# Kernel tuning notes

Measured on AMD Instinct MI355X. Metric: run time of the kernel, lower is better.

The kernel has to match this reference:

```python
import jax, jax.numpy as jnp
import numpy as np

N = 12000       # nodes (Hi-C bins, max_num_nodes)
F_IN = 16       # number_genomic_annotations
HID = 4 * F_IN  # conv1 out = 64
NCLUST = 100    # n_clust
E = 384000      # edges (avg degree 32)


def setup_inputs() -> dict:
    key = jax.random.key(0)
    ks = jax.random.split(key, 8)
    x = jax.random.normal(ks[0], (N, F_IN), dtype=jnp.float32)
    edge_index = jax.random.randint(ks[1], (2, E), 0, N)
    edge_attr = jax.random.uniform(ks[2], (E,), dtype=jnp.float32)
    s1 = 1.0 / np.sqrt(F_IN)
    W1_rel = jax.random.uniform(ks[3], (HID, F_IN), minval=-s1, maxval=s1, dtype=jnp.float32)
    W1_root = jax.random.uniform(ks[4], (HID, F_IN), minval=-s1, maxval=s1, dtype=jnp.float32)
    b1 = jnp.zeros((HID,), jnp.float32)
    s2 = 1.0 / np.sqrt(HID)
    W2_rel = jax.random.uniform(ks[5], (NCLUST, HID), minval=-s2, maxval=s2, dtype=jnp.float32)
    W2_root = jax.random.uniform(ks[6], (NCLUST, HID), minval=-s2, maxval=s2, dtype=jnp.float32)
    b2 = jnp.zeros((NCLUST,), jnp.float32)
    return dict(x=x, edge_index=edge_index, edge_attr=edge_attr,
                W1_rel=W1_rel, W1_root=W1_root, b1=b1,
                W2_rel=W2_rel, W2_root=W2_root, b2=b2)


def _graph_conv(x, src, dst, ew, W_rel, W_root, b):
    # PyG GraphConv (aggr='add'): out = lin_rel(sum_j e_ji * x_j) + lin_root(x)
    msg = x[src] * ew[:, None]                       # [E, F]
    aggr = jax.ops.segment_sum(msg, dst, num_segments=N)  # [N, F]
    return aggr @ W_rel.T + b + x @ W_root.T


def reference(x, edge_index, edge_attr, W1_rel, W1_root, b1, W2_rel, W2_root, b2):
    src, dst = edge_index[0], edge_index[1]
    h = _graph_conv(x, src, dst, edge_attr, W1_rel, W1_root, b1)
    h = jax.nn.relu(h)  # dropout is identity in eval mode
    s_out = _graph_conv(h, src, dst, edge_attr, W2_rel, W2_root, b2)  # [N, NCLUST]

    # to_dense_adj (duplicate edges summed)
    adj = jnp.zeros((N, N), x.dtype).at[src, dst].add(edge_attr)  # [N, N]

    # dense_mincut_pool with S = x (as in the original forward), k = F_IN
    s_mc = jax.nn.softmax(x, axis=-1)      # [N, F_IN]
    as_ = adj @ s_mc                        # [N, F_IN]
    out_adj = s_mc.T @ as_                  # [F_IN, F_IN]
    mincut_num = jnp.trace(out_adj)
    d_flat = adj.sum(-1)                    # [N] degree
    mincut_den = jnp.einsum('ik,i,ik->', s_mc, d_flat, s_mc)  # trace(S^T D S)
    mc = -(mincut_num / mincut_den)

    ss = s_mc.T @ s_mc                      # [F_IN, F_IN]
    i_k = jnp.eye(F_IN, dtype=ss.dtype)
    o = jnp.linalg.norm(ss / jnp.linalg.norm(ss) - i_k / jnp.linalg.norm(i_k))

    return jax.nn.softmax(s_out, axis=-1), mc, o
```

## Files before the change

kernel.cpp:

```cpp
#include <hip/hip_runtime.h>
#include <math.h>

#define N_NODES 12000
#define F_INN 16
#define HIDD 64
#define NCLUST 100
#define NEDGE 384000
#define NBLK_N 47
#define CAP 96
#define EPT 4
#define NBLK_E 375
#define NBLK_F2 (N_NODES / 8)
#define NBIN 188
#define BINW 64
#define BCAP 2560
#define STCAP 24

#define OFF_BINCNT  0
#define OFF_SCAL    188
#define ZERO_ELEMS  190
#define OFF_COUNT   192
#define OFF_SSPART  12192
#define OFF_NORM2   24224
#define OFF_W2TREL  36224
#define OFF_W2TROOT 42624
#define OFF_SMC     49024
#define OFF_H       241024
#define OFF_SRCW    1009024
#define OFF_BINBUF  3313024

__global__ void binA_kernel(const float* __restrict__ x, const int* __restrict__ ei,
                            const float* __restrict__ ew, float* __restrict__ smc,
                            float* __restrict__ norm2, int* __restrict__ bincnt,
                            int2* __restrict__ binbuf, const float* __restrict__ W2_rel,
                            const float* __restrict__ W2_root, float* __restrict__ w2t_rel,
                            float* __restrict__ w2t_root) {
    __shared__ int shmA[188 + 188 * STCAP * 2];
    int t = threadIdx.x;
    int b = blockIdx.x;
    if (b < NBLK_E) {
        int* scnt = shmA;
        int2* sbuf = (int2*)(shmA + 188);
        for (int i = t; i < 188; i += 256) scnt[i] = 0;
        __syncthreads();
        int tid = b * 256 + t;
        int e0 = tid * EPT;
        int4 sv = *(const int4*)(ei + e0);
        int4 dv = *(const int4*)(ei + NEDGE + e0);
        float4 wv = *(const float4*)(ew + e0);
        int s[EPT] = {sv.x, sv.y, sv.z, sv.w};
        int d[EPT] = {dv.x, dv.y, dv.z, dv.w};
        float w[EPT] = {wv.x, wv.y, wv.z, wv.w};
#pragma unroll
        for (int i = 0; i < EPT; ++i) {
            int bin = d[i] >> 6;
            int dl = d[i] & 63;
            int2 rec = make_int2(s[i] | (dl << 16), __float_as_int(w[i]));
            int pos = atomicAdd(&scnt[bin], 1);
            if (pos < STCAP) {
                sbuf[bin * STCAP + pos] = rec;
            } else {
                int base = atomicAdd(&bincnt[bin], 1);
                binbuf[bin * BCAP + base] = rec;
            }
        }
        __syncthreads();
        if (t < 188) {
            int k = scnt[t];
            if (k > STCAP) k = STCAP;
            if (k > 0) {
                int base = atomicAdd(&bincnt[t], k);
                for (int i = 0; i < k; ++i) binbuf[t * BCAP + base + i] = sbuf[t * STCAP + i];
            }
        }
    } else if (b < NBLK_E + NBLK_N) {
        int i = (b - NBLK_E) * 256 + t;
        if (i >= N_NODES) return;
        const float4* xr = (const float4*)(x + i * 16);
        float4 r0 = xr[0], r1 = xr[1], r2 = xr[2], r3 = xr[3];
        float v[16] = {r0.x, r0.y, r0.z, r0.w, r1.x, r1.y, r1.z, r1.w,
                       r2.x, r2.y, r2.z, r2.w, r3.x, r3.y, r3.z, r3.w};
        float m = v[0];
#pragma unroll
        for (int k = 1; k < 16; ++k) m = fmaxf(m, v[k]);
        float s = 0.f;
#pragma unroll
        for (int k = 0; k < 16; ++k) { v[k] = __expf(v[k] - m); s += v[k]; }
        float inv = 1.f / s;
        float n2 = 0.f;
#pragma unroll
        for (int k = 0; k < 16; ++k) { v[k] *= inv; n2 += v[k] * v[k]; }
        float4* so = (float4*)(smc + i * 16);
        so[0] = make_float4(v[0], v[1], v[2], v[3]);
        so[1] = make_float4(v[4], v[5], v[6], v[7]);
        so[2] = make_float4(v[8], v[9], v[10], v[11]);
        so[3] = make_float4(v[12], v[13], v[14], v[15]);
        norm2[i] = n2;
    } else {
        float* fl = (float*)shmA;
        const float* src = (b == NBLK_E + NBLK_N) ? W2_rel : W2_root;
        float* dst = (b == NBLK_E + NBLK_N) ? w2t_rel : w2t_root;
        for (int i = t; i < 6400; i += 256) fl[i] = src[i];
        __syncthreads();
        for (int j = t; j < 6400; j += 256) {
            int kk = j / 100, cl = j - kk * 100;
            dst[j] = fl[cl * 64 + kk];
        }
    }
}

__global__ void binBF1_kernel(const int2* __restrict__ binbuf, const int* __restrict__ bincnt,
                              int* __restrict__ count, int2* __restrict__ srcw,
                              const float* __restrict__ x, const float* __restrict__ W1_rel,
                              const float* __restrict__ W1_root, const float* __restrict__ b1,
                              float* __restrict__ h, const float* __restrict__ smc,
                              float* __restrict__ sspart, const int* __restrict__ ei,
                              const float* __restrict__ ew, const float* __restrict__ norm2,
                              float* __restrict__ scal) {
    __shared__ int shmU[64 + 64 * CAP * 2];
    __shared__ float wrelT[1024], wrootT[1024], b1s[64];
    int t = threadIdx.x;
    int b = blockIdx.x;
    if (b < NBIN) {
        int* cnt = shmU;
        int2* lbuck = (int2*)(shmU + 64);
        for (int idx = t; idx < 1024; idx += 256) {
            int f = idx >> 4, k = idx & 15;
            wrelT[(k << 6) + f]  = W1_rel[idx];
            wrootT[(k << 6) + f] = W1_root[idx];
        }
        if (t < 64) b1s[t] = b1[t];
        for (int i = t; i < 64; i += 256) cnt[i] = 0;
        __syncthreads();
        int nE = bincnt[b];
        const int2* bp = binbuf + b * BCAP;
        for (int i = t; i < nE; i += 256) {
            int2 rec = bp[i];
            int src = rec.x & 0xFFFF;
            int dl = rec.x >> 16;
            int pos = atomicAdd(&cnt[dl], 1);
            if (pos < CAP) lbuck[dl * CAP + pos] = make_int2(src, rec.y);
        }
        __syncthreads();
        int nbase = b * BINW;
        int nvalid = N_NODES - nbase;
        if (nvalid > BINW) nvalid = BINW;
        if (t < nvalid) count[nbase + t] = cnt[t];
        int lim = nvalid * CAP;
        int2* outp = srcw + (size_t)nbase * CAP;
        for (int i = t; i < lim; i += 256) outp[i] = lbuck[i];
        int w = t >> 6, lane = t & 63;
        int j2 = lane >> 2;
        int q  = lane & 3;
        for (int ni = w; ni < nvalid; ni += 4) {
            int n = nbase + ni;
            int len = cnt[ni];
            const int2* bucket = lbuck + ni * CAP;
            float4 acc4 = make_float4(0.f, 0.f, 0.f, 0.f);
            for (int k = 0; k < len; k += 32) {
                int ia = k + j2, ib = k + 16 + j2;
                int2 pa = bucket[ia];
                int2 pb = bucket[ib];
                if (ia >= len) pa = make_int2(0, 0);
                if (ib >= len) pb = make_int2(0, 0);
                float4 va = *(const float4*)(x + pa.x * 16 + q * 4);
                float4 vb = *(const float4*)(x + pb.x * 16 + q * 4);
                float wa = __int_as_float(pa.y), wb = __int_as_float(pb.y);
                acc4.x = fmaf(va.x, wa, acc4.x); acc4.y = fmaf(va.y, wa, acc4.y);
                acc4.z = fmaf(va.z, wa, acc4.z); acc4.w = fmaf(va.w, wa, acc4.w);
                acc4.x = fmaf(vb.x, wb, acc4.x); acc4.y = fmaf(vb.y, wb, acc4.y);
                acc4.z = fmaf(vb.z, wb, acc4.z); acc4.w = fmaf(vb.w, wb, acc4.w);
            }
            acc4.x += __shfl_xor(acc4.x, 4);  acc4.y += __shfl_xor(acc4.y, 4);
            acc4.z += __shfl_xor(acc4.z, 4);  acc4.w += __shfl_xor(acc4.w, 4);
            acc4.x += __shfl_xor(acc4.x, 8);  acc4.y += __shfl_xor(acc4.y, 8);
            acc4.z += __shfl_xor(acc4.z, 8);  acc4.w += __shfl_xor(acc4.w, 8);
            acc4.x += __shfl_xor(acc4.x, 16); acc4.y += __shfl_xor(acc4.y, 16);
            acc4.z += __shfl_xor(acc4.z, 16); acc4.w += __shfl_xor(acc4.w, 16);
            acc4.x += __shfl_xor(acc4.x, 32); acc4.y += __shfl_xor(acc4.y, 32);
            acc4.z += __shfl_xor(acc4.z, 32); acc4.w += __shfl_xor(acc4.w, 32);
            float xv = (lane < 16) ? x[n * 16 + lane] : 0.f;
            float o = b1s[lane];
#define F1STEP(KK, COMP) { float ag = __shfl(acc4.COMP, (KK) >> 2);            \
                           float xb = __shfl(xv, (KK));                        \
                           o = fmaf(ag, wrelT[((KK) << 6) + lane],             \
                                    fmaf(xb, wrootT[((KK) << 6) + lane], o)); }
            F1STEP(0, x)  F1STEP(1, y)  F1STEP(2, z)  F1STEP(3, w)
            F1STEP(4, x)  F1STEP(5, y)  F1STEP(6, z)  F1STEP(7, w)
            F1STEP(8, x)  F1STEP(9, y)  F1STEP(10, z) F1STEP(11, w)
            F1STEP(12, x) F1STEP(13, y) F1STEP(14, z) F1STEP(15, w)
#undef F1STEP
            h[n * 64 + lane] = fmaxf(o, 0.f);
        }
    } else if (b < NBIN + NBLK_N) {
        int bb = b - NBIN;
        float* rows = (float*)shmU;
        int n = bb * 256 + t;
        float* rp = rows + t * 17;
        if (n < N_NODES) {
            const float4* sr = (const float4*)(smc + n * 16);
            float4 a0 = sr[0], a1 = sr[1], a2v = sr[2], a3 = sr[3];
            rp[0] = a0.x;  rp[1] = a0.y;  rp[2] = a0.z;  rp[3] = a0.w;
            rp[4] = a1.x;  rp[5] = a1.y;  rp[6] = a1.z;  rp[7] = a1.w;
            rp[8] = a2v.x; rp[9] = a2v.y; rp[10] = a2v.z; rp[11] = a2v.w;
            rp[12] = a3.x; rp[13] = a3.y; rp[14] = a3.z; rp[15] = a3.w;
        } else {
#pragma unroll
            for (int k = 0; k < 16; ++k) rp[k] = 0.f;
        }
        __syncthreads();
        int a = t & 15, bq = t >> 4;
        float accs = 0.f;
#pragma unroll 4
        for (int r = 0; r < 256; ++r)
            accs = fmaf(rows[r * 17 + a], rows[r * 17 + bq], accs);
        sspart[bb * 256 + t] = accs;
    } else {
        int tid = (b - NBIN - NBLK_N) * 256 + t;
        int e0 = tid * EPT;
        int4 sv = *(const int4*)(ei + e0);
        int4 dv = *(const int4*)(ei + NEDGE + e0);
        float4 wv = *(const float4*)(ew + e0);
        int s[EPT] = {sv.x, sv.y, sv.z, sv.w};
        int d[EPT] = {dv.x, dv.y, dv.z, dv.w};
        float w[EPT] = {wv.x, wv.y, wv.z, wv.w};
        float np = 0.f, dp = 0.f;
#pragma unroll
        for (int i = 0; i < EPT; ++i) {
            const float4* ps = (const float4*)(smc + s[i] * 16);
            const float4* pd = (const float4*)(smc + d[i] * 16);
            float4 s0 = ps[0], s1 = ps[1], s2 = ps[2], s3 = ps[3];
            float4 d0 = pd[0], d1 = pd[1], d2 = pd[2], d3 = pd[3];
            float dot = s0.x * d0.x + s0.y * d0.y + s0.z * d0.z + s0.w * d0.w +
                        s1.x * d1.x + s1.y * d1.y + s1.z * d1.z + s1.w * d1.w +
                        s2.x * d2.x + s2.y * d2.y + s2.z * d2.z + s2.w * d2.w +
                        s3.x * d3.x + s3.y * d3.y + s3.z * d3.z + s3.w * d3.w;
            np = fmaf(w[i], dot, np);
            dp = fmaf(w[i], norm2[s[i]], dp);
        }
        float* redn = (float*)shmU;
        float* redd = (float*)shmU + 256;
        redn[t] = np;
        redd[t] = dp;
        __syncthreads();
        for (int s2 = 128; s2 > 0; s2 >>= 1) {
            if (t < s2) { redn[t] += redn[t + s2]; redd[t] += redd[t + s2]; }
            __syncthreads();
        }
        if (t == 0) {
            atomicAdd(&scal[0], redn[0]);
            atomicAdd(&scal[1], redd[0]);
        }
    }
}

__global__ __launch_bounds__(512) void fused2_finalize_kernel(
    const float* __restrict__ h, const int2* __restrict__ srcw, const int* __restrict__ count,
    const float* __restrict__ w2t_rel, const float* __restrict__ w2t_root,
    const float* __restrict__ b2, float* __restrict__ out, const float* __restrict__ sspart,
    const float* __restrict__ scal) {
    __shared__ float wsrel[6400];
    __shared__ float a2[8][64], hrow[8][64];
    __shared__ float logits[8][104];
    __shared__ float b2s[104];
    int t = threadIdx.x;
    int b = blockIdx.x;
    if (b < NBLK_F2) {
        for (int i = t; i < 6400; i += 512) wsrel[i] = w2t_rel[i];
        if (t < NCLUST) b2s[t] = b2[t];
        int nn = t >> 6;
        int c = t & 63;
        int eslot = c >> 4;
        int q = c & 15;
        int n = b * 8 + nn;
        int len = count[n];
        const int2* bucket = srcw + n * CAP;
        float4 acc4 = make_float4(0.f, 0.f, 0.f, 0.f);
        for (int k = 0; k < len; k += 32) {
            int i0 = k + eslot,      i1 = k + 4 + eslot;
            int i2 = k + 8 + eslot,  i3 = k + 12 + eslot;
            int i4 = k + 16 + eslot, i5 = k + 20 + eslot;
            int i6 = k + 24 + eslot, i7 = k + 28 + eslot;
            int2 pa = bucket[i0]; int2 pb = bucket[i1];
            int2 pc = bucket[i2]; int2 pd = bucket[i3];
            int2 pe = bucket[i4]; int2 pf = bucket[i5];
            int2 pg = bucket[i6]; int2 ph = bucket[i7];
            if (i0 >= len) pa = make_int2(0, 0);
            if (i1 >= len) pb = make_int2(0, 0);
            if (i2 >= len) pc = make_int2(0, 0);
            if (i3 >= len) pd = make_int2(0, 0);
            if (i4 >= len) pe = make_int2(0, 0);
            if (i5 >= len) pf = make_int2(0, 0);
            if (i6 >= len) pg = make_int2(0, 0);
            if (i7 >= len) ph = make_int2(0, 0);
            float4 va = *(const float4*)(h + pa.x * 64 + q * 4);
            float4 vb = *(const float4*)(h + pb.x * 64 + q * 4);
            float4 vc = *(const float4*)(h + pc.x * 64 + q * 4);
            float4 vd = *(const float4*)(h + pd.x * 64 + q * 4);
            float4 ve = *(const float4*)(h + pe.x * 64 + q * 4);
            float4 vf = *(const float4*)(h + pf.x * 64 + q * 4);
            float4 vg = *(const float4*)(h + pg.x * 64 + q * 4);
            float4 vh = *(const float4*)(h + ph.x * 64 + q * 4);
            float wa = __int_as_float(pa.y), wb = __int_as_float(pb.y);
            float wc = __int_as_float(pc.y), wd = __int_as_float(pd.y);
            float we = __int_as_float(pe.y), wf = __int_as_float(pf.y);
            float wg = __int_as_float(pg.y), wh = __int_as_float(ph.y);
            acc4.x = fmaf(va.x, wa, acc4.x); acc4.y = fmaf(va.y, wa, acc4.y);
            acc4.z = fmaf(va.z, wa, acc4.z); acc4.w = fmaf(va.w, wa, acc4.w);
            acc4.x = fmaf(vb.x, wb, acc4.x); acc4.y = fmaf(vb.y, wb, acc4.y);
            acc4.z = fmaf(vb.z, wb, acc4.z); acc4.w = fmaf(vb.w, wb, acc4.w);
            acc4.x = fmaf(vc.x, wc, acc4.x); acc4.y = fmaf(vc.y, wc, acc4.y);
            acc4.z = fmaf(vc.z, wc, acc4.z); acc4.w = fmaf(vc.w, wc, acc4.w);
            acc4.x = fmaf(vd.x, wd, acc4.x); acc4.y = fmaf(vd.y, wd, acc4.y);
            acc4.z = fmaf(vd.z, wd, acc4.z); acc4.w = fmaf(vd.w, wd, acc4.w);
            acc4.x = fmaf(ve.x, we, acc4.x); acc4.y = fmaf(ve.y, we, acc4.y);
            acc4.z = fmaf(ve.z, we, acc4.z); acc4.w = fmaf(ve.w, we, acc4.w);
            acc4.x = fmaf(vf.x, wf, acc4.x); acc4.y = fmaf(vf.y, wf, acc4.y);
            acc4.z = fmaf(vf.z, wf, acc4.z); acc4.w = fmaf(vf.w, wf, acc4.w);
            acc4.x = fmaf(vg.x, wg, acc4.x); acc4.y = fmaf(vg.y, wg, acc4.y);
            acc4.z = fmaf(vg.z, wg, acc4.z); acc4.w = fmaf(vg.w, wg, acc4.w);
            acc4.x = fmaf(vh.x, wh, acc4.x); acc4.y = fmaf(vh.y, wh, acc4.y);
            acc4.z = fmaf(vh.z, wh, acc4.z); acc4.w = fmaf(vh.w, wh, acc4.w);
        }
        acc4.x += __shfl_xor(acc4.x, 16); acc4.y += __shfl_xor(acc4.y, 16);
        acc4.z += __shfl_xor(acc4.z, 16); acc4.w += __shfl_xor(acc4.w, 16);
        acc4.x += __shfl_xor(acc4.x, 32); acc4.y += __shfl_xor(acc4.y, 32);
        acc4.z += __shfl_xor(acc4.z, 32); acc4.w += __shfl_xor(acc4.w, 32);
        if (eslot == 0) *(float4*)(&a2[nn][q * 4]) = acc4;
        hrow[nn][c] = h[n * 64 + c];
        __syncthreads();
        int g = t >> 7, c2 = t & 127;
        if (c2 < NCLUST) {
            int na = 2 * g, nb2 = 2 * g + 1;
            float s0 = b2s[c2], s1 = s0;
#pragma unroll 8
            for (int kk = 0; kk < 64; ++kk) {
                float wr = wsrel[kk * 100 + c2];
                float wo = w2t_root[kk * 100 + c2];
                s0 = fmaf(a2[na][kk], wr, fmaf(hrow[na][kk], wo, s0));
                s1 = fmaf(a2[nb2][kk], wr, fmaf(hrow[nb2][kk], wo, s1));
            }
            logits[na][c2] = s0;
            logits[nb2][c2] = s1;
        }
        __syncthreads();
        float v0 = logits[nn][c];
        float v1 = (c < NCLUST - 64) ? logits[nn][64 + c] : -INFINITY;
        float m = fmaxf(v0, v1);
#pragma unroll
        for (int off = 32; off > 0; off >>= 1) m = fmaxf(m, __shfl_xor(m, off));
        float e0 = __expf(v0 - m);
        float e1 = (c < NCLUST - 64) ? __expf(v1 - m) : 0.f;
        float s = e0 + e1;
#pragma unroll
        for (int off = 32; off > 0; off >>= 1) s += __shfl_xor(s, off);
        float inv = 1.f / s;
        out[n * NCLUST + c] = e0 * inv;
        if (c < NCLUST - 64) out[n * NCLUST + 64 + c] = e1 * inv;
    } else {
        float* red = wsrel;
        float sv = 0.f;
        if (t < 256)
            for (int bb = 0; bb < NBLK_N; ++bb) sv += sspart[bb * 256 + t];
        red[t] = sv * sv;
        __syncthreads();
        for (int s = 256; s > 0; s >>= 1) {
            if (t < s) red[t] += red[t + s];
            __syncthreads();
        }
        float ssnorm = sqrtf(red[0]);
        __syncthreads();
        float diff = (t < 256) ? (sv / ssnorm - ((t % 17 == 0) ? 0.25f : 0.f)) : 0.f;
        red[t] = diff * diff;
        __syncthreads();
        for (int s = 256; s > 0; s >>= 1) {
            if (t < s) red[t] += red[t + s];
            __syncthreads();
        }
        if (t == 0) {
            out[N_NODES * NCLUST + 0] = -(scal[0] / scal[1]);
            out[N_NODES * NCLUST + 1] = sqrtf(red[0]);
        }
    }
}

extern "C" void kernel_launch(void* const* d_in, const int* in_sizes, int n_in,
                              void* d_out, int out_size, void* d_ws, size_t ws_size,
                              hipStream_t stream) {
    const float* x       = (const float*)d_in[0];
    const int*   ei      = (const int*)d_in[1];
    const float* ew      = (const float*)d_in[2];
    const float* W1_rel  = (const float*)d_in[3];
    const float* W1_root = (const float*)d_in[4];
    const float* b1      = (const float*)d_in[5];
    const float* W2_rel  = (const float*)d_in[6];
    const float* W2_root = (const float*)d_in[7];
    const float* b2      = (const float*)d_in[8];
    float* out = (float*)d_out;
    int*   wsi = (int*)d_ws;

    int*   bincnt  = wsi + OFF_BINCNT;
    float* scal    = (float*)(wsi + OFF_SCAL);
    int*   count   = wsi + OFF_COUNT;
    float* sspart  = (float*)(wsi + OFF_SSPART);
    float* norm2   = (float*)(wsi + OFF_NORM2);
    float* w2trel  = (float*)(wsi + OFF_W2TREL);
    float* w2troot = (float*)(wsi + OFF_W2TROOT);
    float* smc     = (float*)(wsi + OFF_SMC);
    float* h       = (float*)(wsi + OFF_H);
    int2*  srcw    = (int2*)(wsi + OFF_SRCW);
    int2*  binbuf  = (int2*)(wsi + OFF_BINBUF);

    hipMemsetAsync(wsi, 0, ZERO_ELEMS * sizeof(int), stream);
    binA_kernel<<<NBLK_E + NBLK_N + 2, 256, 0, stream>>>(x, ei, ew, smc, norm2, bincnt, binbuf,
                                                         W2_rel, W2_root, w2trel, w2troot);
    binBF1_kernel<<<NBIN + NBLK_N + NBLK_E, 256, 0, stream>>>(
        binbuf, bincnt, count, srcw, x, W1_rel, W1_root, b1, h,
        smc, sspart, ei, ew, norm2, scal);
    fused2_finalize_kernel<<<NBLK_F2 + 1, 512, 0, stream>>>(h, srcw, count, w2trel, w2troot,
                                                            b2, out, sspart, scal);
}
```

Baseline: 92.32 us.

## Drop materialized per-node edge buckets; rebuild buckets per 8-node block from bins

Removes the global srcw/count CSR-like bucket arrays. Each 8-node block in both conv kernels now scans its 64-node bin and keeps the edges belonging to its own 8 nodes in shared memory. This cuts global writes and reads of the bucket array and raises parallelism for conv1 from 188 bins to 1500 blocks of 512 threads. The cost is that each bin's records are read 8 times per conv stage, plus atomics on 8 shared counters.

```diff
diff --git a/kernel.cpp b/kernel.cpp
--- a/kernel.cpp
+++ b/kernel.cpp
@@ -8,8 +8,11 @@
 #define NEDGE 384000
 #define NBLK_N 47
 #define CAP 96
+#define LCAP 97
 #define EPT 4
 #define NBLK_E 375
+#define NBLK_F1 (N_NODES / 8)
+#define NBLK_ME 188
 #define NBLK_F2 (N_NODES / 8)
 #define NBIN 188
 #define BINW 64
@@ -19,15 +22,13 @@
 #define OFF_BINCNT  0
 #define OFF_SCAL    188
 #define ZERO_ELEMS  190
-#define OFF_COUNT   192
-#define OFF_SSPART  12192
-#define OFF_NORM2   24224
-#define OFF_W2TREL  36224
-#define OFF_W2TROOT 42624
-#define OFF_SMC     49024
-#define OFF_H       241024
-#define OFF_SRCW    1009024
-#define OFF_BINBUF  3313024
+#define OFF_SSPART  192
+#define OFF_NORM2   12224
+#define OFF_W2TREL  24224
+#define OFF_W2TROOT 30624
+#define OFF_SMC     37024
+#define OFF_H       229024
+#define OFF_BINBUF  997024
 
 __global__ void binA_kernel(const float* __restrict__ x, const int* __restrict__ ei,
                             const float* __restrict__ ew, float* __restrict__ smc,
@@ -109,141 +110,141 @@
     }
 }
 
-__global__ void binBF1_kernel(const int2* __restrict__ binbuf, const int* __restrict__ bincnt,
-                              int* __restrict__ count, int2* __restrict__ srcw,
-                              const float* __restrict__ x, const float* __restrict__ W1_rel,
-                              const float* __restrict__ W1_root, const float* __restrict__ b1,
-                              float* __restrict__ h, const float* __restrict__ smc,
-                              float* __restrict__ sspart, const int* __restrict__ ei,
-                              const float* __restrict__ ew, const float* __restrict__ norm2,
-                              float* __restrict__ scal) {
-    __shared__ int shmU[64 + 64 * CAP * 2];
+__global__ __launch_bounds__(512) void fused1_kernel(
+    const int2* __restrict__ binbuf, const int* __restrict__ bincnt,
+    const float* __restrict__ x, const float* __restrict__ W1_rel,
+    const float* __restrict__ W1_root, const float* __restrict__ b1, float* __restrict__ h,
+    const float* __restrict__ smc, float* __restrict__ sspart, const int* __restrict__ ei,
+    const float* __restrict__ ew, const float* __restrict__ norm2, float* __restrict__ scal) {
+    __shared__ int lb[8 * LCAP * 2 + 8];
     __shared__ float wrelT[1024], wrootT[1024], b1s[64];
+    __shared__ float shm[4352];
     int t = threadIdx.x;
     int b = blockIdx.x;
-    if (b < NBIN) {
-        int* cnt = shmU;
-        int2* lbuck = (int2*)(shmU + 64);
-        for (int idx = t; idx < 1024; idx += 256) {
+    if (b < NBLK_F1) {
+        int2* lbuck = (int2*)lb;
+        int* cnt = lb + 8 * LCAP * 2;
+        for (int idx = t; idx < 1024; idx += 512) {
             int f = idx >> 4, k = idx & 15;
             wrelT[(k << 6) + f]  = W1_rel[idx];
             wrootT[(k << 6) + f] = W1_root[idx];
         }
         if (t < 64) b1s[t] = b1[t];
-        for (int i = t; i < 64; i += 256) cnt[i] = 0;
-        __syncthreads();
-        int nE = bincnt[b];
-        const int2* bp = binbuf + b * BCAP;
-        for (int i = t; i < nE; i += 256) {
+        if (t < 8) cnt[t] = 0;
+        __syncthreads();
+        int bin = b >> 3;
+        int sub = b & 7;
+        int nE = bincnt[bin];
+        const int2* bp = binbuf + bin * BCAP;
+        for (int i = t; i < nE; i += 512) {
             int2 rec = bp[i];
-            int src = rec.x & 0xFFFF;
             int dl = rec.x >> 16;
-            int pos = atomicAdd(&cnt[dl], 1);
-            if (pos < CAP) lbuck[dl * CAP + pos] = make_int2(src, rec.y);
-        }
-        __syncthreads();
-        int nbase = b * BINW;
-        int nvalid = N_NODES - nbase;
-        if (nvalid > BINW) nvalid = BINW;
-        if (t < nvalid) count[nbase + t] = cnt[t];
-        int lim = nvalid * CAP;
-        int2* outp = srcw + (size_t)nbase * CAP;
-        for (int i = t; i < lim; i += 256) outp[i] = lbuck[i];
+            if ((dl >> 3) == sub) {
+                int ln = dl & 7;
+                int pos = atomicAdd(&cnt[ln], 1);
+                if (pos < CAP) lbuck[ln * LCAP + pos] = make_int2(rec.x & 0xFFFF, rec.y);
+            }
+        }
+        __syncthreads();
         int w = t >> 6, lane = t & 63;
         int j2 = lane >> 2;
         int q  = lane & 3;
-        for (int ni = w; ni < nvalid; ni += 4) {
-            int n = nbase + ni;
-            int len = cnt[ni];
-            const int2* bucket = lbuck + ni * CAP;
-            float4 acc4 = make_float4(0.f, 0.f, 0.f, 0.f);
-            for (int k = 0; k < len; k += 32) {
-                int ia = k + j2, ib = k + 16 + j2;
-                int2 pa = bucket[ia];
-                int2 pb = bucket[ib];
-                if (ia >= len) pa = make_int2(0, 0);
-                if (ib >= len) pb = make_int2(0, 0);
-                float4 va = *(const float4*)(x + pa.x * 16 + q * 4);
-                float4 vb = *(const float4*)(x + pb.x * 16 + q * 4);
-                float wa = __int_as_float(pa.y), wb = __int_as_float(pb.y);
-                acc4.x = fmaf(va.x, wa, acc4.x); acc4.y = fmaf(va.y, wa, acc4.y);
-                acc4.z = fmaf(va.z, wa, acc4.z); acc4.w = fmaf(va.w, wa, acc4.w);
-                acc4.x = fmaf(vb.x, wb, acc4.x); acc4.y = fmaf(vb.y, wb, acc4.y);
-                acc4.z = fmaf(vb.z, wb, acc4.z); acc4.w = fmaf(vb.w, wb, acc4.w);
-            }
-            acc4.x += __shfl_xor(acc4.x, 4);  acc4.y += __shfl_xor(acc4.y, 4);
-            acc4.z += __shfl_xor(acc4.z, 4);  acc4.w += __shfl_xor(acc4.w, 4);
-            acc4.x += __shfl_xor(acc4.x, 8);  acc4.y += __shfl_xor(acc4.y, 8);
-            acc4.z += __shfl_xor(acc4.z, 8);  acc4.w += __shfl_xor(acc4.w, 8);
-            acc4.x += __shfl_xor(acc4.x, 16); acc4.y += __shfl_xor(acc4.y, 16);
-            acc4.z += __shfl_xor(acc4.z, 16); acc4.w += __shfl_xor(acc4.w, 16);
-            acc4.x += __shfl_xor(acc4.x, 32); acc4.y += __shfl_xor(acc4.y, 32);
-            acc4.z += __shfl_xor(acc4.z, 32); acc4.w += __shfl_xor(acc4.w, 32);
-            float xv = (lane < 16) ? x[n * 16 + lane] : 0.f;
-            float o = b1s[lane];
+        int n = b * 8 + w;
+        int len = cnt[w];
+        const int2* bucket = lbuck + w * LCAP;
+        float4 acc4 = make_float4(0.f, 0.f, 0.f, 0.f);
+        for (int k = 0; k < len; k += 32) {
+            int ia = k + j2, ib = k + 16 + j2;
+            int2 pa = bucket[ia];
+            int2 pb = bucket[ib];
+            if (ia >= len) pa = make_int2(0, 0);
+            if (ib >= len) pb = make_int2(0, 0);
+            float4 va = *(const float4*)(x + pa.x * 16 + q * 4);
+            float4 vb = *(const float4*)(x + pb.x * 16 + q * 4);
+            float wa = __int_as_float(pa.y), wb = __int_as_float(pb.y);
+            acc4.x = fmaf(va.x, wa, acc4.x); acc4.y = fmaf(va.y, wa, acc4.y);
+            acc4.z = fmaf(va.z, wa, acc4.z); acc4.w = fmaf(va.w, wa, acc4.w);
+            acc4.x = fmaf(vb.x, wb, acc4.x); acc4.y = fmaf(vb.y, wb, acc4.y);
+            acc4.z = fmaf(vb.z, wb, acc4.z); acc4.w = fmaf(vb.w, wb, acc4.w);
+        }
+        acc4.x += __shfl_xor(acc4.x, 4);  acc4.y += __shfl_xor(acc4.y, 4);
+        acc4.z += __shfl_xor(acc4.z, 4);  acc4.w += __shfl_xor(acc4.w, 4);
+        acc4.x += __shfl_xor(acc4.x, 8);  acc4.y += __shfl_xor(acc4.y, 8);
+        acc4.z += __shfl_xor(acc4.z, 8);  acc4.w += __shfl_xor(acc4.w, 8);
+        acc4.x += __shfl_xor(acc4.x, 16); acc4.y += __shfl_xor(acc4.y, 16);
+        acc4.z += __shfl_xor(acc4.z, 16); acc4.w += __shfl_xor(acc4.w, 16);
+        acc4.x += __shfl_xor(acc4.x, 32); acc4.y += __shfl_xor(acc4.y, 32);
+        acc4.z += __shfl_xor(acc4.z, 32); acc4.w += __shfl_xor(acc4.w, 32);
+        float xv = (lane < 16) ? x[n * 16 + lane] : 0.f;
+        float o = b1s[lane];
 #define F1STEP(KK, COMP) { float ag = __shfl(acc4.COMP, (KK) >> 2);            \
                            float xb = __shfl(xv, (KK));                        \
                            o = fmaf(ag, wrelT[((KK) << 6) + lane],             \
                                     fmaf(xb, wrootT[((KK) << 6) + lane], o)); }
-            F1STEP(0, x)  F1STEP(1, y)  F1STEP(2, z)  F1STEP(3, w)
-            F1STEP(4, x)  F1STEP(5, y)  F1STEP(6, z)  F1STEP(7, w)
-            F1STEP(8, x)  F1STEP(9, y)  F1STEP(10, z) F1STEP(11, w)
-            F1STEP(12, x) F1STEP(13, y) F1STEP(14, z) F1STEP(15, w)
+        F1STEP(0, x)  F1STEP(1, y)  F1STEP(2, z)  F1STEP(3, w)
+        F1STEP(4, x)  F1STEP(5, y)  F1STEP(6, z)  F1STEP(7, w)
+        F1STEP(8, x)  F1STEP(9, y)  F1STEP(10, z) F1STEP(11, w)
+        F1STEP(12, x) F1STEP(13, y) F1STEP(14, z) F1STEP(15, w)
 #undef F1STEP
-            h[n * 64 + lane] = fmaxf(o, 0.f);
-        }
-    } else if (b < NBIN + NBLK_N) {
-        int bb = b - NBIN;
-        float* rows = (float*)shmU;
+        h[n * 64 + lane] = fmaxf(o, 0.f);
+    } else if (b < NBLK_F1 + NBLK_N) {
+        int bb = b - NBLK_F1;
+        float* rows = shm;
         int n = bb * 256 + t;
-        float* rp = rows + t * 17;
-        if (n < N_NODES) {
-            const float4* sr = (const float4*)(smc + n * 16);
-            float4 a0 = sr[0], a1 = sr[1], a2v = sr[2], a3 = sr[3];
-            rp[0] = a0.x;  rp[1] = a0.y;  rp[2] = a0.z;  rp[3] = a0.w;
-            rp[4] = a1.x;  rp[5] = a1.y;  rp[6] = a1.z;  rp[7] = a1.w;
-            rp[8] = a2v.x; rp[9] = a2v.y; rp[10] = a2v.z; rp[11] = a2v.w;
-            rp[12] = a3.x; rp[13] = a3.y; rp[14] = a3.z; rp[15] = a3.w;
-        } else {
-#pragma unroll
-            for (int k = 0; k < 16; ++k) rp[k] = 0.f;
-        }
-        __syncthreads();
-        int a = t & 15, bq = t >> 4;
-        float accs = 0.f;
+        if (t < 256) {
+            float* rp = rows + t * 17;
+            if (n < N_NODES) {
+                const float4* sr = (const float4*)(smc + n * 16);
+                float4 a0 = sr[0], a1 = sr[1], a2v = sr[2], a3 = sr[3];
+                rp[0] = a0.x;  rp[1] = a0.y;  rp[2] = a0.z;  rp[3] = a0.w;
+                rp[4] = a1.x;  rp[5] = a1.y;  rp[6] = a1.z;  rp[7] = a1.w;
+                rp[8] = a2v.x; rp[9] = a2v.y; rp[10] = a2v.z; rp[11] = a2v.w;
+                rp[12] = a3.x; rp[13] = a3.y; rp[14] = a3.z; rp[15] = a3.w;
+            } else {
+#pragma unroll
+                for (int k = 0; k < 16; ++k) rp[k] = 0.f;
+            }
+        }
+        __syncthreads();
+        if (t < 256) {
+            int a = t & 15, bq = t >> 4;
+            float accs = 0.f;
 #pragma unroll 4
-        for (int r = 0; r < 256; ++r)
-            accs = fmaf(rows[r * 17 + a], rows[r * 17 + bq], accs);
-        sspart[bb * 256 + t] = accs;
+            for (int r = 0; r < 256; ++r)
+                accs = fmaf(rows[r * 17 + a], rows[r * 17 + bq], accs);
+            sspart[bb * 256 + t] = accs;
+        }
     } else {
-        int tid = (b - NBIN - NBLK_N) * 256 + t;
+        int tid = (b - NBLK_F1 - NBLK_N) * 512 + t;
         int e0 = tid * EPT;
-        int4 sv = *(const int4*)(ei + e0);
-        int4 dv = *(const int4*)(ei + NEDGE + e0);
-        float4 wv = *(const float4*)(ew + e0);
-        int s[EPT] = {sv.x, sv.y, sv.z, sv.w};
-        int d[EPT] = {dv.x, dv.y, dv.z, dv.w};
-        float w[EPT] = {wv.x, wv.y, wv.z, wv.w};
         float np = 0.f, dp = 0.f;
-#pragma unroll
-        for (int i = 0; i < EPT; ++i) {
-            const float4* ps = (const float4*)(smc + s[i] * 16);
-            const float4* pd = (const float4*)(smc + d[i] * 16);
-            float4 s0 = ps[0], s1 = ps[1], s2 = ps[2], s3 = ps[3];
-            float4 d0 = pd[0], d1 = pd[1], d2 = pd[2], d3 = pd[3];
-            float dot = s0.x * d0.x + s0.y * d0.y + s0.z * d0.z + s0.w * d0.w +
-                        s1.x * d1.x + s1.y * d1.y + s1.z * d1.z + s1.w * d1.w +
-                        s2.x * d2.x + s2.y * d2.y + s2.z * d2.z + s2.w * d2.w +
-                        s3.x * d3.x + s3.y * d3.y + s3.z * d3.z + s3.w * d3.w;
-            np = fmaf(w[i], dot, np);
-            dp = fmaf(w[i], norm2[s[i]], dp);
-        }
-        float* redn = (float*)shmU;
-        float* redd = (float*)shmU + 256;
+        if (e0 < NEDGE) {
+            int4 sv = *(const int4*)(ei + e0);
+            int4 dv = *(const int4*)(ei + NEDGE + e0);
+            float4 wv = *(const float4*)(ew + e0);
+            int s[EPT] = {sv.x, sv.y, sv.z, sv.w};
+            int d[EPT] = {dv.x, dv.y, dv.z, dv.w};
+            float w[EPT] = {wv.x, wv.y, wv.z, wv.w};
+#pragma unroll
+            for (int i = 0; i < EPT; ++i) {
+                const float4* ps = (const float4*)(smc + s[i] * 16);
+                const float4* pd = (const float4*)(smc + d[i] * 16);
+                float4 s0 = ps[0], s1 = ps[1], s2 = ps[2], s3 = ps[3];
+                float4 d0 = pd[0], d1 = pd[1], d2 = pd[2], d3 = pd[3];
+                float dot = s0.x * d0.x + s0.y * d0.y + s0.z * d0.z + s0.w * d0.w +
+                            s1.x * d1.x + s1.y * d1.y + s1.z * d1.z + s1.w * d1.w +
+                            s2.x * d2.x + s2.y * d2.y + s2.z * d2.z + s2.w * d2.w +
+                            s3.x * d3.x + s3.y * d3.y + s3.z * d3.z + s3.w * d3.w;
+                np = fmaf(w[i], dot, np);
+                dp = fmaf(w[i], norm2[s[i]], dp);
+            }
+        }
+        float* redn = shm;
+        float* redd = shm + 512;
         redn[t] = np;
         redd[t] = dp;
         __syncthreads();
-        for (int s2 = 128; s2 > 0; s2 >>= 1) {
+        for (int s2 = 256; s2 > 0; s2 >>= 1) {
             if (t < s2) { redn[t] += redn[t + s2]; redd[t] += redd[t + s2]; }
             __syncthreads();
         }
@@ -255,26 +256,45 @@
 }
 
 __global__ __launch_bounds__(512) void fused2_finalize_kernel(
-    const float* __restrict__ h, const int2* __restrict__ srcw, const int* __restrict__ count,
-    const float* __restrict__ w2t_rel, const float* __restrict__ w2t_root,
-    const float* __restrict__ b2, float* __restrict__ out, const float* __restrict__ sspart,
-    const float* __restrict__ scal) {
+    const int2* __restrict__ binbuf, const int* __restrict__ bincnt,
+    const float* __restrict__ h, const float* __restrict__ w2t_rel,
+    const float* __restrict__ w2t_root, const float* __restrict__ b2, float* __restrict__ out,
+    const float* __restrict__ sspart, const float* __restrict__ scal) {
     __shared__ float wsrel[6400];
+    __shared__ int lb[8 * LCAP * 2 + 8];
     __shared__ float a2[8][64], hrow[8][64];
     __shared__ float logits[8][104];
     __shared__ float b2s[104];
     int t = threadIdx.x;
     int b = blockIdx.x;
     if (b < NBLK_F2) {
+        int2* lbuck = (int2*)lb;
+        int* cnt = lb + 8 * LCAP * 2;
         for (int i = t; i < 6400; i += 512) wsrel[i] = w2t_rel[i];
         if (t < NCLUST) b2s[t] = b2[t];
+        if (t < 8) cnt[t] = 0;
+        __syncthreads();
+        int bin = b >> 3;
+        int sub = b & 7;
+        int nE = bincnt[bin];
+        const int2* bp = binbuf + bin * BCAP;
+        for (int i = t; i < nE; i += 512) {
+            int2 rec = bp[i];
+            int dl = rec.x >> 16;
+            if ((dl >> 3) == sub) {
+                int ln = dl & 7;
+                int pos = atomicAdd(&cnt[ln], 1);
+                if (pos < CAP) lbuck[ln * LCAP + pos] = make_int2(rec.x & 0xFFFF, rec.y);
+            }
+        }
+        __syncthreads();
         int nn = t >> 6;
         int c = t & 63;
         int eslot = c >> 4;
         int q = c & 15;
         int n = b * 8 + nn;
-        int len = count[n];
-        const int2* bucket = srcw + n * CAP;
+        int len = cnt[nn];
+        const int2* bucket = lbuck + nn * LCAP;
         float4 acc4 = make_float4(0.f, 0.f, 0.f, 0.f);
         for (int k = 0; k < len; k += 32) {
             int i0 = k + eslot,      i1 = k + 4 + eslot;
@@ -401,22 +421,19 @@
 
     int*   bincnt  = wsi + OFF_BINCNT;
     float* scal    = (float*)(wsi + OFF_SCAL);
-    int*   count   = wsi + OFF_COUNT;
     float* sspart  = (float*)(wsi + OFF_SSPART);
     float* norm2   = (float*)(wsi + OFF_NORM2);
     float* w2trel  = (float*)(wsi + OFF_W2TREL);
     float* w2troot = (float*)(wsi + OFF_W2TROOT);
     float* smc     = (float*)(wsi + OFF_SMC);
     float* h       = (float*)(wsi + OFF_H);
-    int2*  srcw    = (int2*)(wsi + OFF_SRCW);
     int2*  binbuf  = (int2*)(wsi + OFF_BINBUF);
 
     hipMemsetAsync(wsi, 0, ZERO_ELEMS * sizeof(int), stream);
     binA_kernel<<<NBLK_E + NBLK_N + 2, 256, 0, stream>>>(x, ei, ew, smc, norm2, bincnt, binbuf,
                                                          W2_rel, W2_root, w2trel, w2troot);
-    binBF1_kernel<<<NBIN + NBLK_N + NBLK_E, 256, 0, stream>>>(
-        binbuf, bincnt, count, srcw, x, W1_rel, W1_root, b1, h,
-        smc, sspart, ei, ew, norm2, scal);
-    fused2_finalize_kernel<<<NBLK_F2 + 1, 512, 0, stream>>>(h, srcw, count, w2trel, w2troot,
+    fused1_kernel<<<NBLK_F1 + NBLK_N + NBLK_ME, 512, 0, stream>>>(
+        binbuf, bincnt, x, W1_rel, W1_root, b1, h, smc, sspart, ei, ew, norm2, scal);
+    fused2_finalize_kernel<<<NBLK_F2 + 1, 512, 0, stream>>>(binbuf, bincnt, h, w2trel, w2troot,
                                                             b2, out, sspart, scal);
 }
```

Result: faster. 88.30 us (-4.4%).
